# Kernel tuning notes

Hardware: AMD Instinct MI355X
Metric: run time of the kernel (lower is better)

The kernel has to match this reference:

```python
import jax, jax.numpy as jnp
import numpy as np

N_NODES = 1_000_000
N_EDGES = 10_000_000
HIDDEN = 8
N_GRAPHS = 64


def _gcn_conv(h_in, W, b, src, dst, deg_inv_sqrt, n_nodes):
    """One PyG GCNConv: symmetric-normalized aggregation over (A + I)."""
    h = h_in @ W  # [N, out]
    norm = deg_inv_sqrt[src] * deg_inv_sqrt[dst]  # [E]
    msgs = h[src] * norm[:, None]  # gather + scale, [E, out]
    out = jax.ops.segment_sum(msgs, dst, num_segments=n_nodes)  # scatter-add
    out = out + h * (deg_inv_sqrt * deg_inv_sqrt)[:, None]  # self-loop term
    return out + b


def setup_inputs() -> dict:
    key = jax.random.key(0)
    ks = jax.random.split(key, 12)
    x = jax.random.uniform(ks[0], (N_NODES, 1), dtype=jnp.float32)
    edge_index = jax.random.randint(ks[1], (2, N_EDGES), 0, N_NODES, dtype=jnp.int64)
    indices = jax.random.randint(ks[2], (N_GRAPHS,), 0, N_NODES, dtype=jnp.int64)
    # Glorot-ish init for GCNConv linear layers (no bias in lin; GCNConv bias separate)
    W1 = jax.random.normal(ks[3], (1, HIDDEN), dtype=jnp.float32) * (1.0 / np.sqrt(1))
    W2 = jax.random.normal(ks[4], (HIDDEN, HIDDEN), dtype=jnp.float32) * (1.0 / np.sqrt(HIDDEN))
    W3 = jax.random.normal(ks[5], (HIDDEN, HIDDEN), dtype=jnp.float32) * (1.0 / np.sqrt(HIDDEN))
    W4 = jax.random.normal(ks[6], (HIDDEN, HIDDEN), dtype=jnp.float32) * (1.0 / np.sqrt(HIDDEN))
    b1 = jnp.zeros((HIDDEN,), jnp.float32)
    b2 = jnp.zeros((HIDDEN,), jnp.float32)
    b3 = jnp.zeros((HIDDEN,), jnp.float32)
    b4 = jnp.zeros((HIDDEN,), jnp.float32)
    return {"x": x, "edge_index": edge_index, "indices": indices,
            "W1": W1, "b1": b1, "W2": W2, "b2": b2,
            "W3": W3, "b3": b3, "W4": W4, "b4": b4}


def reference(x, edge_index, indices, W1, b1, W2, b2, W3, b3, W4, b4):
    n_nodes = x.shape[0]
    src, dst = edge_index[0], edge_index[1]
    # degree under A + I (symmetric GCN normalization)
    deg = jax.ops.segment_sum(jnp.ones_like(dst, dtype=x.dtype), dst,
                              num_segments=n_nodes) + 1.0
    deg_inv_sqrt = jax.lax.rsqrt(deg)
    h = x
    for W, b, last in ((W1, b1, False), (W2, b2, False), (W3, b3, False), (W4, b4, True)):
        h = _gcn_conv(h, W, b, src, dst, deg_inv_sqrt, n_nodes)
        if not last:
            h = jax.nn.relu(h)
    return h[indices]  # one node embedding per batched graph, [B, 8]
```

## Files before the change

### kernel.cpp

```cpp
#include <hip/hip_runtime.h>
#include <hip/hip_fp16.h>

#define TPB 256
#define STPB 512
#define BTPB 512
#define NBK 256
#define BNODES 4096
#define QNODES 1024
#define CH 6144
#define CAPB 45056
#define QSTG 12288
#define CAP_L 262144

typedef unsigned int uv4 __attribute__((ext_vector_type(4)));
union H8 { uv4 u; __half2 h2[4]; };

__global__ __launch_bounds__(STPB) void scatter_sort(const int* __restrict__ dst,
                                                     const int* __restrict__ src,
                                                     int* __restrict__ tails,
                                                     unsigned* __restrict__ bdata, int nE) {
    __shared__ unsigned      stage[CH];
    __shared__ unsigned char bkt[CH];
    __shared__ int cnt[NBK], sstart[NBK], cur[NBK], cbase[NBK];
    __shared__ int wsum[STPB / 64];
    int t = threadIdx.x;
    long base = (long)blockIdx.x * CH;
    int m = (int)(((long)nE - base < CH) ? (nE - base) : CH);
    if (t < NBK) cnt[t] = 0;
    __syncthreads();
    for (int k = t * 4; k < m; k += STPB * 4) {
        if (k + 3 < m) {
            int4 d4 = *(const int4*)(dst + base + k);
            atomicAdd(&cnt[d4.x >> 12], 1);
            atomicAdd(&cnt[d4.y >> 12], 1);
            atomicAdd(&cnt[d4.z >> 12], 1);
            atomicAdd(&cnt[d4.w >> 12], 1);
        } else {
            int ke = (k + 4 < m) ? (k + 4) : m;
            for (int kk = k; kk < ke; ++kk)
                atomicAdd(&cnt[dst[base + kk] >> 12], 1);
        }
    }
    __syncthreads();
    int v = 0, incl = 0;
    if (t < NBK) {
        v = cnt[t]; incl = v;
#pragma unroll
        for (int o = 1; o < 64; o <<= 1) {
            int u = __shfl_up(incl, o, 64);
            if ((t & 63) >= o) incl += u;
        }
        if ((t & 63) == 63) wsum[t >> 6] = incl;
    }
    __syncthreads();
    if (t < NBK) {
        int wadd = 0;
#pragma unroll
        for (int w = 0; w < 3; ++w) wadd += (w < (t >> 6)) ? wsum[w] : 0;
        int ex = incl - v + wadd;
        sstart[t] = ex;
        cur[t] = ex;
        cbase[t] = v ? (t * CAPB + atomicAdd(&tails[t], v)) : 0;
    }
    __syncthreads();
    for (int k = t * 4; k < m; k += STPB * 4) {
        if (k + 3 < m) {
            int4 d4 = *(const int4*)(dst + base + k);
            int4 s4 = *(const int4*)(src + base + k);
            { int b = d4.x >> 12; int pos = atomicAdd(&cur[b], 1);
              stage[pos] = ((unsigned)(d4.x & 4095) << 20) | (unsigned)s4.x; bkt[pos] = (unsigned char)b; }
            { int b = d4.y >> 12; int pos = atomicAdd(&cur[b], 1);
              stage[pos] = ((unsigned)(d4.y & 4095) << 20) | (unsigned)s4.y; bkt[pos] = (unsigned char)b; }
            { int b = d4.z >> 12; int pos = atomicAdd(&cur[b], 1);
              stage[pos] = ((unsigned)(d4.z & 4095) << 20) | (unsigned)s4.z; bkt[pos] = (unsigned char)b; }
            { int b = d4.w >> 12; int pos = atomicAdd(&cur[b], 1);
              stage[pos] = ((unsigned)(d4.w & 4095) << 20) | (unsigned)s4.w; bkt[pos] = (unsigned char)b; }
        } else {
            int ke = (k + 4 < m) ? (k + 4) : m;
            for (int kk = k; kk < ke; ++kk) {
                int d = dst[base + kk], s = src[base + kk];
                int b = d >> 12; int pos = atomicAdd(&cur[b], 1);
                stage[pos] = ((unsigned)(d & 4095) << 20) | (unsigned)s; bkt[pos] = (unsigned char)b;
            }
        }
    }
    __syncthreads();
    for (int k = t; k < m; k += STPB) {
        int b = bkt[k];
        bdata[cbase[b] + (k - sstart[b])] = stage[k];
    }
}

__global__ __launch_bounds__(BTPB) void quarter_csr(const unsigned* __restrict__ bdata,
                                                    const int* __restrict__ tails,
                                                    const float* __restrict__ x,
                                                    const float* __restrict__ W1,
                                                    int* __restrict__ rowptr,
                                                    __half* __restrict__ hs,
                                                    int* __restrict__ col, int n, int NB) {
    __shared__ int      off[QNODES];
    __shared__ int      wsum[BTPB / 64];
    __shared__ int      wredQ[BTPB / 64];
    __shared__ int      wredP[BTPB / 64];
    __shared__ int      sQb, sTot, sPb;
    __shared__ unsigned stg[QSTG];
    int bid = blockIdx.x, t = threadIdx.x;
    int xcd = bid & 7, slot = bid >> 3;
    int b = (slot >> 2) * 8 + xcd;
    int q = slot & 3;
    if (b >= NB) return;
    int e0 = b * CAPB, e1 = e0 + tails[b];
    for (int j = t; j < QNODES; j += BTPB) off[j] = 0;
    int partial = (t < b) ? tails[t] : 0;
#pragma unroll
    for (int o = 32; o > 0; o >>= 1) partial += __shfl_down(partial, o, 64);
    if ((t & 63) == 0) wredP[t >> 6] = partial;
    __syncthreads();
    if (t == 0) {
        int s = 0;
#pragma unroll
        for (int w = 0; w < BTPB / 64; ++w) s += wredP[w];
        sPb = s;
    }
    int before = 0;
    for (int k = e0 + t * 4; k < e1; k += BTPB * 4) {
        if (k + 3 < e1) {
            uv4 p4 = *(const uv4*)(bdata + k);
#pragma unroll
            for (int z = 0; z < 4; ++z) {
                int j = (int)(p4[z] >> 20); int jq = j >> 10;
                if (jq == q) atomicAdd(&off[j & 1023], 1);
                before += (jq < q) ? 1 : 0;
            }
        } else {
            for (int kk = k; kk < e1; ++kk) {
                int j = (int)(bdata[kk] >> 20); int jq = j >> 10;
                if (jq == q) atomicAdd(&off[j & 1023], 1);
                before += (jq < q) ? 1 : 0;
            }
        }
    }
#pragma unroll
    for (int o = 32; o > 0; o >>= 1) before += __shfl_down(before, o, 64);
    if ((t & 63) == 0) wredQ[t >> 6] = before;
    __syncthreads();
    if (t == 0) {
        int s = 0;
#pragma unroll
        for (int w = 0; w < BTPB / 64; ++w) s += wredQ[w];
        sQb = s;
    }
    int a = off[2 * t], c = off[2 * t + 1];
    int s2 = a + c;
    int incl = s2;
#pragma unroll
    for (int o = 1; o < 64; o <<= 1) {
        int u = __shfl_up(incl, o, 64);
        if ((t & 63) >= o) incl += u;
    }
    if ((t & 63) == 63) wsum[t >> 6] = incl;
    __syncthreads();
    int wadd = 0;
#pragma unroll
    for (int w = 0; w < BTPB / 64 - 1; ++w) wadd += (w < (t >> 6)) ? wsum[w] : 0;
    int pex = incl - s2 + wadd;
    off[2 * t]     = pex;
    off[2 * t + 1] = pex + a;
    if (t == BTPB - 1) sTot = pex + s2;
    int PbQb = sPb + sQb;
    {
        int node0 = (b << 12) + (q << 10) + 2 * t;
        float4 w0 = ((const float4*)W1)[0];
        float4 w1 = ((const float4*)W1)[1];
        if (node0 + 1 < n) {
            int2 rp; rp.x = PbQb + pex; rp.y = PbQb + pex + a;
            *(int2*)(rowptr + node0) = rp;
            float2 xv = *(const float2*)(x + node0);
            float dv0 = rsqrtf((float)a + 1.0f);
            float dv1 = rsqrtf((float)c + 1.0f);
            float xd0 = xv.x * dv0, xd1 = xv.y * dv1;
            H8 o0, o1;
            o0.h2[0] = __floats2half2_rn(xd0 * w0.x, xd0 * w0.y);
            o0.h2[1] = __floats2half2_rn(xd0 * w0.z, xd0 * w0.w);
            o0.h2[2] = __floats2half2_rn(xd0 * w1.x, xd0 * w1.y);
            o0.h2[3] = __floats2half2_rn(xd0 * w1.z, xd0 * w1.w);
            o1.h2[0] = __floats2half2_rn(xd1 * w0.x, xd1 * w0.y);
            o1.h2[1] = __floats2half2_rn(xd1 * w0.z, xd1 * w0.w);
            o1.h2[2] = __floats2half2_rn(xd1 * w1.x, xd1 * w1.y);
            o1.h2[3] = __floats2half2_rn(xd1 * w1.z, xd1 * w1.w);
            ((uv4*)hs)[node0]     = o0.u;
            ((uv4*)hs)[node0 + 1] = o1.u;
        } else {
            if (node0 <= n)     rowptr[node0]     = PbQb + pex;
            if (node0 + 1 <= n) rowptr[node0 + 1] = PbQb + pex + a;
            if (node0 < n) {
                float dv = rsqrtf((float)a + 1.0f);
                float xd = x[node0] * dv;
                H8 o;
                o.h2[0] = __floats2half2_rn(xd * w0.x, xd * w0.y);
                o.h2[1] = __floats2half2_rn(xd * w0.z, xd * w0.w);
                o.h2[2] = __floats2half2_rn(xd * w1.x, xd * w1.y);
                o.h2[3] = __floats2half2_rn(xd * w1.z, xd * w1.w);
                ((uv4*)hs)[node0] = o.u;
            }
        }
    }
    __syncthreads();
    for (int k = e0 + t * 4; k < e1; k += BTPB * 4) {
        if (k + 3 < e1) {
            uv4 p4 = *(const uv4*)(bdata + k);
#pragma unroll
            for (int z = 0; z < 4; ++z) {
                int j = (int)(p4[z] >> 20);
                if ((j >> 10) == q) {
                    int pos = atomicAdd(&off[j & 1023], 1);
                    stg[pos] = p4[z] & 0xFFFFFu;
                }
            }
        } else {
            for (int kk = k; kk < e1; ++kk) {
                unsigned p = bdata[kk];
                int j = (int)(p >> 20);
                if ((j >> 10) == q) {
                    int pos = atomicAdd(&off[j & 1023], 1);
                    stg[pos] = p & 0xFFFFFu;
                }
            }
        }
    }
    __syncthreads();
    int tot = sTot;
    for (int k = t; k < tot; k += BTPB)
        col[PbQb + k] = (int)stg[k];
}

__global__ void seed_mark_q(const int* __restrict__ idx, int B, int* __restrict__ mark,
                            int* __restrict__ L, int* __restrict__ qq) {
    int t = threadIdx.x;
    if (t < B) {
        int u = idx[t];
        if (atomicCAS(&mark[u], 0, 1) == 0)
            L[atomicAdd(&qq[7], 1)] = u;
    }
}

__global__ __launch_bounds__(TPB) void expand_f(int* __restrict__ L, int* __restrict__ qq,
                                                int tier,
                                                const int* __restrict__ rowptr,
                                                const int* __restrict__ col,
                                                int* __restrict__ mark) {
    int hi = qq[7];
    int stride = gridDim.x * blockDim.x;
    int lane = threadIdx.x & 63;
    for (int r = blockIdx.x * blockDim.x + threadIdx.x; r < hi; r += stride) {
        int u = L[r];
        if (mark[u] != tier - 1) continue;
        int e0 = rowptr[u], e1 = rowptr[u + 1];
        for (int k = e0; k < e1; ++k) {
            int s = col[k];
            bool ok = (mark[s] == 0) && (atomicCAS(&mark[s], 0, tier) == 0);
            unsigned long long msk = __ballot(ok);
            if (msk) {
                int leader = __builtin_ctzll(msk);
                int cntw = __builtin_popcountll(msk);
                int basep = 0;
                if (lane == leader) basep = atomicAdd(&qq[7], cntw);
                basep = __shfl(basep, leader, 64);
                if (ok) {
                    int myoff = __builtin_popcountll(msk & ((1ull << lane) - 1ull));
                    L[basep + myoff] = s;
                }
            }
        }
    }
}

__global__ __launch_bounds__(TPB) void pull_tier(const int* __restrict__ L,
                          const int* __restrict__ qq,
                          int tagMax, const int* __restrict__ mark,
                          const int* __restrict__ rowptr, const int* __restrict__ col,
                          const __half* __restrict__ hs_in, const float* __restrict__ bias,
                          const float* __restrict__ W, __half* __restrict__ hs_out) {
    int gidx = blockIdx.x * blockDim.x + threadIdx.x;
    int r = gidx >> 2;
    int sl = gidx & 3;
    if (r >= qq[7]) return;
    int u = L[r];
    if (mark[u] > tagMax) return;
    const uv4* hv = (const uv4*)hs_in;
    float2 a0 = {0.f, 0.f}, a1 = {0.f, 0.f}, a2 = {0.f, 0.f}, a3 = {0.f, 0.f};
    int s = rowptr[u], e = rowptr[u + 1];
    for (int k = s + sl; k < e; k += 4) {
        H8 q; q.u = hv[col[k]];
        float2 b0 = __half22float2(q.h2[0]);
        float2 b1 = __half22float2(q.h2[1]);
        float2 b2 = __half22float2(q.h2[2]);
        float2 b3 = __half22float2(q.h2[3]);
        a0.x += b0.x; a0.y += b0.y; a1.x += b1.x; a1.y += b1.y;
        a2.x += b2.x; a2.y += b2.y; a3.x += b3.x; a3.y += b3.y;
    }
#pragma unroll
    for (int o = 1; o <= 2; o <<= 1) {
        a0.x += __shfl_xor(a0.x, o, 64); a0.y += __shfl_xor(a0.y, o, 64);
        a1.x += __shfl_xor(a1.x, o, 64); a1.y += __shfl_xor(a1.y, o, 64);
        a2.x += __shfl_xor(a2.x, o, 64); a2.y += __shfl_xor(a2.y, o, 64);
        a3.x += __shfl_xor(a3.x, o, 64); a3.y += __shfl_xor(a3.y, o, 64);
    }
    if (sl != 0) return;
    H8 p; p.u = hv[u];
    float2 s0 = __half22float2(p.h2[0]);
    float2 s1 = __half22float2(p.h2[1]);
    float2 s2 = __half22float2(p.h2[2]);
    float2 s3 = __half22float2(p.h2[3]);
    a0.x += s0.x; a0.y += s0.y; a1.x += s1.x; a1.y += s1.y;
    a2.x += s2.x; a2.y += s2.y; a3.x += s3.x; a3.y += s3.y;
    float d = rsqrtf((float)(e - s) + 1.0f);
    float t[8] = {a0.x * d, a0.y * d, a1.x * d, a1.y * d,
                  a2.x * d, a2.y * d, a3.x * d, a3.y * d};
#pragma unroll
    for (int k = 0; k < 8; ++k) {
        float v = t[k] + bias[k];
        t[k] = v > 0.0f ? v : 0.0f;
    }
    float h[8];
#pragma unroll
    for (int j = 0; j < 8; ++j) {
        float acc = 0.0f;
#pragma unroll
        for (int k = 0; k < 8; ++k) acc += t[k] * W[k * 8 + j];
        h[j] = acc * d;
    }
    H8 o;
    o.h2[0] = __floats2half2_rn(h[0], h[1]);
    o.h2[1] = __floats2half2_rn(h[2], h[3]);
    o.h2[2] = __floats2half2_rn(h[4], h[5]);
    o.h2[3] = __floats2half2_rn(h[6], h[7]);
    ((uv4*)hs_out)[u] = o.u;
}

__global__ void pull_final(const int* __restrict__ idx, int B,
                           const int* __restrict__ rowptr, const int* __restrict__ col,
                           const __half* __restrict__ hs_in,
                           const float* __restrict__ b4, float* __restrict__ out) {
    int t = blockIdx.x * blockDim.x + threadIdx.x;
    if (t >= B) return;
    int u = idx[t];
    const uv4* hv = (const uv4*)hs_in;
    H8 p; p.u = hv[u];
    float2 a0 = __half22float2(p.h2[0]);
    float2 a1 = __half22float2(p.h2[1]);
    float2 a2 = __half22float2(p.h2[2]);
    float2 a3 = __half22float2(p.h2[3]);
    int s = rowptr[u], e = rowptr[u + 1];
    for (int k = s; k < e; ++k) {
        H8 q; q.u = hv[col[k]];
        float2 b0 = __half22float2(q.h2[0]);
        float2 b1 = __half22float2(q.h2[1]);
        float2 b2 = __half22float2(q.h2[2]);
        float2 b3 = __half22float2(q.h2[3]);
        a0.x += b0.x; a0.y += b0.y; a1.x += b1.x; a1.y += b1.y;
        a2.x += b2.x; a2.y += b2.y; a3.x += b3.x; a3.y += b3.y;
    }
    float d = rsqrtf((float)(e - s) + 1.0f);
    float* op = out + (size_t)t * 8;
    op[0] = a0.x * d + b4[0]; op[1] = a0.y * d + b4[1];
    op[2] = a1.x * d + b4[2]; op[3] = a1.y * d + b4[3];
    op[4] = a2.x * d + b4[4]; op[5] = a2.y * d + b4[5];
    op[6] = a3.x * d + b4[6]; op[7] = a3.y * d + b4[7];
}

extern "C" void kernel_launch(void* const* d_in, const int* in_sizes, int n_in,
                              void* d_out, int out_size, void* d_ws, size_t ws_size,
                              hipStream_t stream) {
    const float* x   = (const float*)d_in[0];
    const int*   ei  = (const int*)d_in[1];
    const int*   idx = (const int*)d_in[2];
    const float* W1  = (const float*)d_in[3];
    const float* b1  = (const float*)d_in[4];
    const float* W2  = (const float*)d_in[5];
    const float* b2  = (const float*)d_in[6];
    const float* W3  = (const float*)d_in[7];
    const float* b3  = (const float*)d_in[8];
    const float* W4  = (const float*)d_in[9];
    const float* b4  = (const float*)d_in[10];

    const int n = in_sizes[0];
    const int E = in_sizes[1] / 2;
    const int B = in_sizes[2];

    const int* src = ei;
    const int* dst = ei + E;

    const int NB = (n + BNODES - 1) / BNODES;

    size_t o_mark = 0;
    size_t o_rp   = o_mark + (size_t)n;
    size_t o_hsA  = o_rp   + (size_t)n + 8;
    size_t o_L    = o_hsA  + (size_t)n * 4;
    size_t o_col  = o_L    + CAP_L;
    size_t o_bd   = o_col  + (size_t)E;
    size_t o_sm   = o_bd   + (size_t)NB * CAPB;

    int*      mark   = (int*)d_ws + o_mark;
    int*      rowptr = (int*)d_ws + o_rp;
    __half*   hsA    = (__half*)((int*)d_ws + o_hsA);
    int*      L      = (int*)d_ws + o_L;
    int*      col    = (int*)d_ws + o_col;
    unsigned* bdata  = (unsigned*)((int*)d_ws + o_bd);
    __half*   hsB    = (__half*)bdata;
    int*      tails  = (int*)d_ws + o_sm;
    int*      qq     = tails + NBK;

    const int gs  = (int)(((long)E + CH - 1) / CH);
    const int nb4 = (CAP_L * 4) / TPB;
    const int gq  = ((NB + 7) / 8) * 32;

    (void)hipMemsetAsync(mark, 0, (size_t)n * sizeof(int), stream);
    (void)hipMemsetAsync(tails, 0, (NBK + 16) * sizeof(int), stream);

    scatter_sort<<<gs, STPB, 0, stream>>>(dst, src, tails, bdata, E);

    quarter_csr<<<gq, BTPB, 0, stream>>>(bdata, tails, x, W1, rowptr, hsA, col, n, NB);

    seed_mark_q<<<1, 64, 0, stream>>>(idx, B, mark, L, qq);
    expand_f<<<64, TPB, 0, stream>>>(L, qq, 2, rowptr, col, mark);
    expand_f<<<128, TPB, 0, stream>>>(L, qq, 3, rowptr, col, mark);
    expand_f<<<256, TPB, 0, stream>>>(L, qq, 4, rowptr, col, mark);

    pull_tier<<<nb4, TPB, 0, stream>>>(L, qq, 4, mark, rowptr, col, hsA, b1, W2, hsB);
    pull_tier<<<nb4, TPB, 0, stream>>>(L, qq, 3, mark, rowptr, col, hsB, b2, W3, hsA);
    pull_tier<<<nb4, TPB, 0, stream>>>(L, qq, 2, mark, rowptr, col, hsA, b3, W4, hsB);
    pull_final<<<1, 64, 0, stream>>>(idx, B, rowptr, col, hsB, b4, (float*)d_out);
}
```

Measured before the change: 380.5 us.

## Use per-wave bucket counters in scatter sort and grid-stride pull tiers

scatter_sort now keeps a histogram and write cursor per wave and bucket instead of block-wide ones, and drops the per-element bucket byte array. The flush to global memory becomes a contiguous copy per bucket, one wave per bucket. pull_tier becomes a grid-stride loop with smaller per-tier grids and skips the mark read at the outermost tier. The two memsets are merged into one by making the tails/qq buffers contiguous with mark. The aim is less LDS atomic contention, coalesced bucket writes and fewer idle threads launched, at the cost of more LDS for counters.

```diff
diff --git a/kernel.cpp b/kernel.cpp
--- a/kernel.cpp
+++ b/kernel.cpp
@@ -3,6 +3,7 @@
 
 #define TPB 256
 #define STPB 512
+#define NW 8
 #define BTPB 512
 #define NBK 256
 #define BNODES 4096
@@ -19,32 +20,36 @@
                                                      const int* __restrict__ src,
                                                      int* __restrict__ tails,
                                                      unsigned* __restrict__ bdata, int nE) {
-    __shared__ unsigned      stage[CH];
-    __shared__ unsigned char bkt[CH];
-    __shared__ int cnt[NBK], sstart[NBK], cur[NBK], cbase[NBK];
-    __shared__ int wsum[STPB / 64];
+    __shared__ unsigned stage[CH];
+    __shared__ int      cnt8[NW * NBK];
+    __shared__ int      cnt[NBK], sstart[NBK], cbase[NBK];
+    __shared__ int      wsum[STPB / 64];
     int t = threadIdx.x;
+    int w = t >> 6;
     long base = (long)blockIdx.x * CH;
     int m = (int)(((long)nE - base < CH) ? (nE - base) : CH);
-    if (t < NBK) cnt[t] = 0;
+    for (int j = t; j < NW * NBK; j += STPB) cnt8[j] = 0;
     __syncthreads();
     for (int k = t * 4; k < m; k += STPB * 4) {
         if (k + 3 < m) {
             int4 d4 = *(const int4*)(dst + base + k);
-            atomicAdd(&cnt[d4.x >> 12], 1);
-            atomicAdd(&cnt[d4.y >> 12], 1);
-            atomicAdd(&cnt[d4.z >> 12], 1);
-            atomicAdd(&cnt[d4.w >> 12], 1);
+            atomicAdd(&cnt8[w * NBK + (d4.x >> 12)], 1);
+            atomicAdd(&cnt8[w * NBK + (d4.y >> 12)], 1);
+            atomicAdd(&cnt8[w * NBK + (d4.z >> 12)], 1);
+            atomicAdd(&cnt8[w * NBK + (d4.w >> 12)], 1);
         } else {
             int ke = (k + 4 < m) ? (k + 4) : m;
             for (int kk = k; kk < ke; ++kk)
-                atomicAdd(&cnt[dst[base + kk] >> 12], 1);
+                atomicAdd(&cnt8[w * NBK + (dst[base + kk] >> 12)], 1);
         }
     }
     __syncthreads();
     int v = 0, incl = 0;
     if (t < NBK) {
-        v = cnt[t]; incl = v;
+        v = 0;
+#pragma unroll
+        for (int ww = 0; ww < NW; ++ww) v += cnt8[ww * NBK + t];
+        incl = v;
 #pragma unroll
         for (int o = 1; o < 64; o <<= 1) {
             int u = __shfl_up(incl, o, 64);
@@ -56,38 +61,47 @@
     if (t < NBK) {
         int wadd = 0;
 #pragma unroll
-        for (int w = 0; w < 3; ++w) wadd += (w < (t >> 6)) ? wsum[w] : 0;
+        for (int ww = 0; ww < 3; ++ww) wadd += (ww < (t >> 6)) ? wsum[ww] : 0;
         int ex = incl - v + wadd;
         sstart[t] = ex;
-        cur[t] = ex;
+        cnt[t] = v;
         cbase[t] = v ? (t * CAPB + atomicAdd(&tails[t], v)) : 0;
+        int run = ex;
+#pragma unroll
+        for (int ww = 0; ww < NW; ++ww) {
+            int tmp = cnt8[ww * NBK + t];
+            cnt8[ww * NBK + t] = run;
+            run += tmp;
+        }
     }
     __syncthreads();
     for (int k = t * 4; k < m; k += STPB * 4) {
         if (k + 3 < m) {
             int4 d4 = *(const int4*)(dst + base + k);
             int4 s4 = *(const int4*)(src + base + k);
-            { int b = d4.x >> 12; int pos = atomicAdd(&cur[b], 1);
-              stage[pos] = ((unsigned)(d4.x & 4095) << 20) | (unsigned)s4.x; bkt[pos] = (unsigned char)b; }
-            { int b = d4.y >> 12; int pos = atomicAdd(&cur[b], 1);
-              stage[pos] = ((unsigned)(d4.y & 4095) << 20) | (unsigned)s4.y; bkt[pos] = (unsigned char)b; }
-            { int b = d4.z >> 12; int pos = atomicAdd(&cur[b], 1);
-              stage[pos] = ((unsigned)(d4.z & 4095) << 20) | (unsigned)s4.z; bkt[pos] = (unsigned char)b; }
-            { int b = d4.w >> 12; int pos = atomicAdd(&cur[b], 1);
-              stage[pos] = ((unsigned)(d4.w & 4095) << 20) | (unsigned)s4.w; bkt[pos] = (unsigned char)b; }
+            { int pos = atomicAdd(&cnt8[w * NBK + (d4.x >> 12)], 1);
+              stage[pos] = ((unsigned)(d4.x & 4095) << 20) | (unsigned)s4.x; }
+            { int pos = atomicAdd(&cnt8[w * NBK + (d4.y >> 12)], 1);
+              stage[pos] = ((unsigned)(d4.y & 4095) << 20) | (unsigned)s4.y; }
+            { int pos = atomicAdd(&cnt8[w * NBK + (d4.z >> 12)], 1);
+              stage[pos] = ((unsigned)(d4.z & 4095) << 20) | (unsigned)s4.z; }
+            { int pos = atomicAdd(&cnt8[w * NBK + (d4.w >> 12)], 1);
+              stage[pos] = ((unsigned)(d4.w & 4095) << 20) | (unsigned)s4.w; }
         } else {
             int ke = (k + 4 < m) ? (k + 4) : m;
             for (int kk = k; kk < ke; ++kk) {
                 int d = dst[base + kk], s = src[base + kk];
-                int b = d >> 12; int pos = atomicAdd(&cur[b], 1);
-                stage[pos] = ((unsigned)(d & 4095) << 20) | (unsigned)s; bkt[pos] = (unsigned char)b;
-            }
-        }
-    }
-    __syncthreads();
-    for (int k = t; k < m; k += STPB) {
-        int b = bkt[k];
-        bdata[cbase[b] + (k - sstart[b])] = stage[k];
+                int pos = atomicAdd(&cnt8[w * NBK + (d >> 12)], 1);
+                stage[pos] = ((unsigned)(d & 4095) << 20) | (unsigned)s;
+            }
+        }
+    }
+    __syncthreads();
+    int lane = t & 63;
+    for (int b2 = w; b2 < NBK; b2 += NW) {
+        int c = cnt[b2], s0 = sstart[b2], g0 = cbase[b2];
+        for (int k = lane; k < c; k += 64)
+            bdata[g0 + k] = stage[s0 + k];
     }
 }
 
@@ -281,61 +295,64 @@
                           const int* __restrict__ rowptr, const int* __restrict__ col,
                           const __half* __restrict__ hs_in, const float* __restrict__ bias,
                           const float* __restrict__ W, __half* __restrict__ hs_out) {
-    int gidx = blockIdx.x * blockDim.x + threadIdx.x;
-    int r = gidx >> 2;
-    int sl = gidx & 3;
-    if (r >= qq[7]) return;
-    int u = L[r];
-    if (mark[u] > tagMax) return;
+    int nrows = qq[7];
+    int gstride = gridDim.x * blockDim.x;
     const uv4* hv = (const uv4*)hs_in;
-    float2 a0 = {0.f, 0.f}, a1 = {0.f, 0.f}, a2 = {0.f, 0.f}, a3 = {0.f, 0.f};
-    int s = rowptr[u], e = rowptr[u + 1];
-    for (int k = s + sl; k < e; k += 4) {
-        H8 q; q.u = hv[col[k]];
-        float2 b0 = __half22float2(q.h2[0]);
-        float2 b1 = __half22float2(q.h2[1]);
-        float2 b2 = __half22float2(q.h2[2]);
-        float2 b3 = __half22float2(q.h2[3]);
-        a0.x += b0.x; a0.y += b0.y; a1.x += b1.x; a1.y += b1.y;
-        a2.x += b2.x; a2.y += b2.y; a3.x += b3.x; a3.y += b3.y;
-    }
-#pragma unroll
-    for (int o = 1; o <= 2; o <<= 1) {
-        a0.x += __shfl_xor(a0.x, o, 64); a0.y += __shfl_xor(a0.y, o, 64);
-        a1.x += __shfl_xor(a1.x, o, 64); a1.y += __shfl_xor(a1.y, o, 64);
-        a2.x += __shfl_xor(a2.x, o, 64); a2.y += __shfl_xor(a2.y, o, 64);
-        a3.x += __shfl_xor(a3.x, o, 64); a3.y += __shfl_xor(a3.y, o, 64);
-    }
-    if (sl != 0) return;
-    H8 p; p.u = hv[u];
-    float2 s0 = __half22float2(p.h2[0]);
-    float2 s1 = __half22float2(p.h2[1]);
-    float2 s2 = __half22float2(p.h2[2]);
-    float2 s3 = __half22float2(p.h2[3]);
-    a0.x += s0.x; a0.y += s0.y; a1.x += s1.x; a1.y += s1.y;
-    a2.x += s2.x; a2.y += s2.y; a3.x += s3.x; a3.y += s3.y;
-    float d = rsqrtf((float)(e - s) + 1.0f);
-    float t[8] = {a0.x * d, a0.y * d, a1.x * d, a1.y * d,
-                  a2.x * d, a2.y * d, a3.x * d, a3.y * d};
-#pragma unroll
-    for (int k = 0; k < 8; ++k) {
-        float v = t[k] + bias[k];
-        t[k] = v > 0.0f ? v : 0.0f;
-    }
-    float h[8];
-#pragma unroll
-    for (int j = 0; j < 8; ++j) {
-        float acc = 0.0f;
-#pragma unroll
-        for (int k = 0; k < 8; ++k) acc += t[k] * W[k * 8 + j];
-        h[j] = acc * d;
-    }
-    H8 o;
-    o.h2[0] = __floats2half2_rn(h[0], h[1]);
-    o.h2[1] = __floats2half2_rn(h[2], h[3]);
-    o.h2[2] = __floats2half2_rn(h[4], h[5]);
-    o.h2[3] = __floats2half2_rn(h[6], h[7]);
-    ((uv4*)hs_out)[u] = o.u;
+    for (int gidx = blockIdx.x * blockDim.x + threadIdx.x; (gidx >> 2) < nrows;
+         gidx += gstride) {
+        int r = gidx >> 2;
+        int sl = gidx & 3;
+        int u = L[r];
+        if (tagMax < 4 && mark[u] > tagMax) continue;
+        float2 a0 = {0.f, 0.f}, a1 = {0.f, 0.f}, a2 = {0.f, 0.f}, a3 = {0.f, 0.f};
+        int s = rowptr[u], e = rowptr[u + 1];
+        for (int k = s + sl; k < e; k += 4) {
+            H8 q; q.u = hv[col[k]];
+            float2 b0 = __half22float2(q.h2[0]);
+            float2 b1 = __half22float2(q.h2[1]);
+            float2 b2 = __half22float2(q.h2[2]);
+            float2 b3 = __half22float2(q.h2[3]);
+            a0.x += b0.x; a0.y += b0.y; a1.x += b1.x; a1.y += b1.y;
+            a2.x += b2.x; a2.y += b2.y; a3.x += b3.x; a3.y += b3.y;
+        }
+#pragma unroll
+        for (int o = 1; o <= 2; o <<= 1) {
+            a0.x += __shfl_xor(a0.x, o, 64); a0.y += __shfl_xor(a0.y, o, 64);
+            a1.x += __shfl_xor(a1.x, o, 64); a1.y += __shfl_xor(a1.y, o, 64);
+            a2.x += __shfl_xor(a2.x, o, 64); a2.y += __shfl_xor(a2.y, o, 64);
+            a3.x += __shfl_xor(a3.x, o, 64); a3.y += __shfl_xor(a3.y, o, 64);
+        }
+        if (sl != 0) continue;
+        H8 p; p.u = hv[u];
+        float2 s0 = __half22float2(p.h2[0]);
+        float2 s1 = __half22float2(p.h2[1]);
+        float2 s2 = __half22float2(p.h2[2]);
+        float2 s3 = __half22float2(p.h2[3]);
+        a0.x += s0.x; a0.y += s0.y; a1.x += s1.x; a1.y += s1.y;
+        a2.x += s2.x; a2.y += s2.y; a3.x += s3.x; a3.y += s3.y;
+        float d = rsqrtf((float)(e - s) + 1.0f);
+        float t[8] = {a0.x * d, a0.y * d, a1.x * d, a1.y * d,
+                      a2.x * d, a2.y * d, a3.x * d, a3.y * d};
+#pragma unroll
+        for (int k = 0; k < 8; ++k) {
+            float v = t[k] + bias[k];
+            t[k] = v > 0.0f ? v : 0.0f;
+        }
+        float h[8];
+#pragma unroll
+        for (int j = 0; j < 8; ++j) {
+            float acc = 0.0f;
+#pragma unroll
+            for (int k = 0; k < 8; ++k) acc += t[k] * W[k * 8 + j];
+            h[j] = acc * d;
+        }
+        H8 o;
+        o.h2[0] = __floats2half2_rn(h[0], h[1]);
+        o.h2[1] = __floats2half2_rn(h[2], h[3]);
+        o.h2[2] = __floats2half2_rn(h[4], h[5]);
+        o.h2[3] = __floats2half2_rn(h[6], h[7]);
+        ((uv4*)hs_out)[u] = o.u;
+    }
 }
 
 __global__ void pull_final(const int* __restrict__ idx, int B,
@@ -393,30 +410,29 @@
 
     const int NB = (n + BNODES - 1) / BNODES;
 
-    size_t o_mark = 0;
-    size_t o_rp   = o_mark + (size_t)n;
-    size_t o_hsA  = o_rp   + (size_t)n + 8;
-    size_t o_L    = o_hsA  + (size_t)n * 4;
-    size_t o_col  = o_L    + CAP_L;
-    size_t o_bd   = o_col  + (size_t)E;
-    size_t o_sm   = o_bd   + (size_t)NB * CAPB;
+    size_t o_mark  = 0;
+    size_t o_tails = o_mark  + (size_t)n;
+    size_t o_qq    = o_tails + NBK;
+    size_t o_rp    = o_qq    + 16;
+    size_t o_hsA   = o_rp    + (size_t)n + 8;
+    size_t o_L     = o_hsA   + (size_t)n * 4;
+    size_t o_col   = o_L     + CAP_L;
+    size_t o_bd    = o_col   + (size_t)E;
 
     int*      mark   = (int*)d_ws + o_mark;
+    int*      tails  = (int*)d_ws + o_tails;
+    int*      qq     = (int*)d_ws + o_qq;
     int*      rowptr = (int*)d_ws + o_rp;
     __half*   hsA    = (__half*)((int*)d_ws + o_hsA);
     int*      L      = (int*)d_ws + o_L;
     int*      col    = (int*)d_ws + o_col;
     unsigned* bdata  = (unsigned*)((int*)d_ws + o_bd);
     __half*   hsB    = (__half*)bdata;
-    int*      tails  = (int*)d_ws + o_sm;
-    int*      qq     = tails + NBK;
 
     const int gs  = (int)(((long)E + CH - 1) / CH);
-    const int nb4 = (CAP_L * 4) / TPB;
     const int gq  = ((NB + 7) / 8) * 32;
 
-    (void)hipMemsetAsync(mark, 0, (size_t)n * sizeof(int), stream);
-    (void)hipMemsetAsync(tails, 0, (NBK + 16) * sizeof(int), stream);
+    (void)hipMemsetAsync(mark, 0, ((size_t)n + NBK + 16) * sizeof(int), stream);
 
     scatter_sort<<<gs, STPB, 0, stream>>>(dst, src, tails, bdata, E);
 
@@ -427,8 +443,8 @@
     expand_f<<<128, TPB, 0, stream>>>(L, qq, 3, rowptr, col, mark);
     expand_f<<<256, TPB, 0, stream>>>(L, qq, 4, rowptr, col, mark);
 
-    pull_tier<<<nb4, TPB, 0, stream>>>(L, qq, 4, mark, rowptr, col, hsA, b1, W2, hsB);
-    pull_tier<<<nb4, TPB, 0, stream>>>(L, qq, 3, mark, rowptr, col, hsB, b2, W3, hsA);
-    pull_tier<<<nb4, TPB, 0, stream>>>(L, qq, 2, mark, rowptr, col, hsA, b3, W4, hsB);
+    pull_tier<<<2048, TPB, 0, stream>>>(L, qq, 4, mark, rowptr, col, hsA, b1, W2, hsB);
+    pull_tier<<<256,  TPB, 0, stream>>>(L, qq, 3, mark, rowptr, col, hsB, b2, W3, hsA);
+    pull_tier<<<64,   TPB, 0, stream>>>(L, qq, 2, mark, rowptr, col, hsA, b3, W4, hsB);
     pull_final<<<1, 64, 0, stream>>>(idx, B, rowptr, col, hsB, b4, (float*)d_out);
 }
```

After: 371.2 us. 1.03x faster.
